# Kernel tuning notes

Measured on AMD Instinct MI355X. Metric: run time of the kernel, lower is better.

## Reference

```python
import jax, jax.numpy as jnp
import numpy as np

DIM = 640
HEADS = 8
HEAD_DIM = 80
CROSS = 768
FF_INNER = 4 * DIM  # 2560
EPS = 1e-5
SCALE = HEAD_DIM ** -0.5


def _ln(x, w, b):
    m = jnp.mean(x, axis=-1, keepdims=True)
    v = jnp.var(x, axis=-1, keepdims=True)
    return (x - m) * jax.lax.rsqrt(v + EPS) * w + b


def _split_heads(x):  # [B,S,D] -> [B,H,S,dh]
    B, S, D = x.shape
    return x.reshape(B, S, HEADS, D // HEADS).transpose(0, 2, 1, 3)


def _merge_heads(x):  # [B,H,S,dh] -> [B,S,D]
    B, H, S, dh = x.shape
    return x.transpose(0, 2, 1, 3).reshape(B, S, H * dh)


def _mha(q, k, v):
    # q:[B,S,D] k,v:[B,Skv,D]
    qh, kh, vh = _split_heads(q), _split_heads(k), _split_heads(v)
    scores = jnp.einsum('bhqd,bhkd->bhqk', qh, kh) * SCALE
    probs = jax.nn.softmax(scores, axis=-1)
    out = jnp.einsum('bhqk,bhkd->bhqd', probs, vh)
    return _merge_heads(out)


def _forward(hidden_states, encoder_hidden_states, video_length, p):
    BF, S, D = hidden_states.shape
    f = video_length
    b = BF // f

    # ---- attn1: sparse causal self-attention ----
    x = _ln(hidden_states, p['ln1_w'], p['ln1_b'])
    q = x @ p['q1']
    k = x @ p['k1']
    v = x @ p['v1']
    former = jnp.concatenate([jnp.zeros((1,), jnp.int32), jnp.arange(f - 1, dtype=jnp.int32)])
    def gather_kv(t):  # [BF,S,D] -> [BF,2S,D]
        t = t.reshape(b, f, S, D)
        first = jnp.broadcast_to(t[:, 0:1], (b, f, S, D))
        prev = t[:, former]
        return jnp.concatenate([first, prev], axis=2).reshape(BF, 2 * S, D)
    k = gather_kv(k)
    v = gather_kv(v)
    attn1 = _mha(q, k, v) @ p['o1_w'] + p['o1_b']
    hidden_states = attn1 + hidden_states

    # ---- attn2: cross attention to text ----
    x = _ln(hidden_states, p['ln2_w'], p['ln2_b'])
    q = x @ p['q2']
    k = encoder_hidden_states @ p['k2']
    v = encoder_hidden_states @ p['v2']
    attn2 = _mha(q, k, v) @ p['o2_w'] + p['o2_b']
    hidden_states = attn2 + hidden_states

    # ---- feed-forward (geglu) ----
    x = _ln(hidden_states, p['ln3_w'], p['ln3_b'])
    proj = x @ p['ff_w1'] + p['ff_b1']
    h, gate = jnp.split(proj, 2, axis=-1)
    ff = (h * jax.nn.gelu(gate)) @ p['ff_w2'] + p['ff_b2']
    return ff + hidden_states


def setup_inputs() -> dict:
    key = jax.random.key(0)
    ks = jax.random.split(key, 20)
    s = lambda i, shape, scale=0.02: jax.random.normal(ks[i], shape, jnp.float32) * scale
    inp = {
        'hidden_states': jax.random.normal(ks[0], (8, 1024, DIM), jnp.float32),
        'encoder_hidden_states': jax.random.normal(ks[1], (8, 77, CROSS), jnp.float32),
        'video_length': 8,
        'ln1_w': jnp.ones((DIM,)), 'ln1_b': jnp.zeros((DIM,)),
        'q1': s(2, (DIM, DIM)), 'k1': s(3, (DIM, DIM)), 'v1': s(4, (DIM, DIM)),
        'o1_w': s(5, (DIM, DIM)), 'o1_b': jnp.zeros((DIM,)),
        'ln2_w': jnp.ones((DIM,)), 'ln2_b': jnp.zeros((DIM,)),
        'q2': s(6, (DIM, DIM)), 'k2': s(7, (CROSS, DIM)), 'v2': s(8, (CROSS, DIM)),
        'o2_w': s(9, (DIM, DIM)), 'o2_b': jnp.zeros((DIM,)),
        'ln3_w': jnp.ones((DIM,)), 'ln3_b': jnp.zeros((DIM,)),
        'ff_w1': s(10, (DIM, 2 * FF_INNER)), 'ff_b1': jnp.zeros((2 * FF_INNER,)),
        'ff_w2': s(11, (FF_INNER, DIM)), 'ff_b2': jnp.zeros((DIM,)),
    }
    return inp


def reference(hidden_states, encoder_hidden_states, video_length,
              ln1_w, ln1_b, q1, k1, v1, o1_w, o1_b,
              ln2_w, ln2_b, q2, k2, v2, o2_w, o2_b,
              ln3_w, ln3_b, ff_w1, ff_b1, ff_w2, ff_b2):
    p = dict(ln1_w=ln1_w, ln1_b=ln1_b, q1=q1, k1=k1, v1=v1, o1_w=o1_w, o1_b=o1_b,
             ln2_w=ln2_w, ln2_b=ln2_b, q2=q2, k2=k2, v2=v2, o2_w=o2_w, o2_b=o2_b,
             ln3_w=ln3_w, ln3_b=ln3_b, ff_w1=ff_w1, ff_b1=ff_b1, ff_w2=ff_w2, ff_b2=ff_b2)
    return _forward(hidden_states, encoder_hidden_states, video_length, p)
```

## Files before the change

### kernel.cpp

```cpp
#include <hip/hip_runtime.h>
#include <stdint.h>

#define TOK   8192
#define DIM   640
#define HEADS 8
#define HD    80
#define SEQ   1024
#define CROSS 768
#define ETOK  616
#define FFI   2560
#define SCALE 0.11180339887498949f

typedef unsigned short u16;
typedef unsigned int   u32;

using bf8   = __attribute__((ext_vector_type(8))) short;
using f32x4 = __attribute__((ext_vector_type(4))) float;

struct __align__(16) U4 { u32 x, y, z, w; };
struct __align__(8)  U2 { u32 x, y; };

__device__ __forceinline__ float bf2f(u16 u){
  union { u32 i; float f; } v; v.i = ((u32)u) << 16; return v.f;
}
__device__ __forceinline__ u16 f2bf(float f){
  union { float f; u32 i; } v; v.f = f;
  u32 r = v.i + 0x7fffu + ((v.i >> 16) & 1u);
  return (u16)(r >> 16);
}
__device__ __forceinline__ u32 cvtpk_bf16(float lo, float hi){
  u32 r; asm("v_cvt_pk_bf16_f32 %0, %1, %2" : "=v"(r) : "v"(lo), "v"(hi)); return r;
}
__device__ __forceinline__ float gelu_t(float x){
  float y = 0.7978845608028654f * (x + 0.044715f * x * x * x);
  float e = __expf(2.f * y);
  return 0.5f * x * (2.f - 2.f / (e + 1.f));
}

__device__ __forceinline__ void gl2lds16(const u16* g, u16* l){
  __builtin_amdgcn_global_load_lds(
      (const __attribute__((address_space(1))) void*)g,
      (__attribute__((address_space(3))) void*)l, 16, 0, 0);
}

__global__ void zero_k(u16* p){ p[threadIdx.x] = 0; }

struct CvtJob  { const float* s; u16* d; int n; };
struct CvtJobs { CvtJob j[11]; };
__global__ __launch_bounds__(256) void cvt_all(CvtJobs jobs)
{
  const CvtJob jb = jobs.j[blockIdx.y];
  for (long i = (long)blockIdx.x*256 + threadIdx.x; i < jb.n; i += (long)gridDim.x*256)
    jb.d[i] = f2bf(jb.s[i]);
}

struct TJob  { const float* s; u16* d; int R, C, srcLd, dstLd; };
struct TJobs { TJob j[10]; };
__global__ __launch_bounds__(256) void transpose_tiled(TJobs jobs)
{
  const TJob jb = jobs.j[blockIdx.y];
  const int tilesC = jb.C >> 6;
  const int nt = (jb.R >> 6) * tilesC;
  if ((int)blockIdx.x >= nt) return;
  const int tr = (blockIdx.x / tilesC) << 6, tc = (blockIdx.x % tilesC) << 6;
  __shared__ u16 t[64][65];
  const int tid = threadIdx.x;
  const int rr = tid >> 3, c8 = (tid & 7) * 8;
  #pragma unroll
  for (int p = 0; p < 2; ++p){
    const int r = rr + p*32;
    const float* s = &jb.s[(long)(tr + r)*jb.srcLd + tc + c8];
    #pragma unroll
    for (int j = 0; j < 8; ++j) t[r][c8 + j] = f2bf(s[j]);
  }
  __syncthreads();
  #pragma unroll
  for (int p = 0; p < 2; ++p){
    const int c = rr + p*32;
    u16 tmp[8];
    #pragma unroll
    for (int j = 0; j < 8; ++j) tmp[j] = t[c8 + j][c];
    *(U4*)&jb.d[(long)(tc + c)*jb.dstLd + tr + c8] = *(U4*)tmp;
  }
}

__global__ __launch_bounds__(256) void transpose_tile(
    const u16* __restrict__ src, u16* __restrict__ dst,
    int srcLd, int dstLd)
{
  __shared__ u16 t[64][65];
  const int tr = blockIdx.y << 6, tc = blockIdx.x << 6;
  const int tid = threadIdx.x;
  const int rr = tid >> 3, c8 = (tid & 7) * 8;
  #pragma unroll
  for (int p = 0; p < 2; ++p){
    const int r = rr + p*32;
    U4 v = *(const U4*)&src[(long)(tr + r)*srcLd + tc + c8];
    const u16* pv = (const u16*)&v;
    #pragma unroll
    for (int j = 0; j < 8; ++j) t[r][c8 + j] = pv[j];
  }
  __syncthreads();
  #pragma unroll
  for (int p = 0; p < 2; ++p){
    const int c = rr + p*32;
    u16 tmp[8];
    #pragma unroll
    for (int j = 0; j < 8; ++j) tmp[j] = t[c8 + j][c];
    *(U4*)&dst[(long)(tc + c)*dstLd + tr + c8] = *(U4*)tmp;
  }
}

__global__ __launch_bounds__(256) void transpose_v2(
    const u16* __restrict__ src, u16* __restrict__ dst)
{
  int idx = blockIdx.x*256 + threadIdx.x;
  if (idx >= DIM*640) return;
  int d = idx / 640, c = idx - d*640;
  int g = c / 80, j = c - g*80;
  u16 v = 0;
  if (j < 77) v = src[(long)(g*77 + j)*(2*DIM) + DIM + d];
  dst[(long)d*640 + c] = v;
}

__global__ __launch_bounds__(256) void ln_k(
    const void* __restrict__ src, const u16* __restrict__ w,
    const u16* __restrict__ b, u16* __restrict__ dst, int srcf32)
{
  __shared__ float xr[DIM];
  __shared__ float red[256];
  const int tid = threadIdx.x;
  const long row = blockIdx.x;
  float ls = 0.f;
  for (int i = tid; i < DIM; i += 256){
    float v = srcf32 ? ((const float*)src)[row*DIM + i]
                     : bf2f(((const u16*)src)[row*DIM + i]);
    xr[i] = v; ls += v;
  }
  red[tid] = ls; __syncthreads();
  for (int o = 128; o > 0; o >>= 1){ if (tid < o) red[tid] += red[tid+o]; __syncthreads(); }
  const float mean = red[0] * (1.f/DIM);
  __syncthreads();
  float lq = 0.f;
  for (int i = tid; i < DIM; i += 256){ float d = xr[i] - mean; lq += d*d; }
  red[tid] = lq; __syncthreads();
  for (int o = 128; o > 0; o >>= 1){ if (tid < o) red[tid] += red[tid+o]; __syncthreads(); }
  const float var = red[0] * (1.f/DIM);
  const float rs = rsqrtf(var + 1e-5f);
  u16* q = dst + row*DIM;
  for (int i = tid; i < DIM; i += 256)
    q[i] = f2bf((xr[i] - mean)*rs*bf2f(w[i]) + bf2f(b[i]));
}

template<int BN>
__global__ __launch_bounds__(256) void gemm_bt(
    const u16* __restrict__ A, const u16* __restrict__ BT, void* __restrict__ C,
    int M, int N, int K, int lda, int ldb, int ldc,
    const u16* __restrict__ bias, const void* __restrict__ res, int ldr,
    int resf32, int outf32)
{
  constexpr int NT  = BN/32;
  constexpr int BCH = BN/16;
  constexpr int BPW = BCH/4;
  __shared__ __align__(16) u16 sA[2][8*512];
  __shared__ __align__(16) u16 sB[2][BCH*512];
  const int tid  = threadIdx.x;
  const int wave = tid >> 6, lane = tid & 63;
  const int quad = lane >> 4, l16 = lane & 15;
  const int m0 = blockIdx.y * 128, n0 = blockIdx.x * BN;
  const int wm = (wave >> 1) * 64, wn = (wave & 1) * (BN/2);
  const int srow = lane & 15;
  const int scol = (lane >> 4) * 8;

  long aoff[2];
  #pragma unroll
  for (int i = 0; i < 2; ++i){
    int r = m0 + (wave*2 + i)*16 + srow;
    r = r < M ? r : M - 1;
    aoff[i] = (long)r*lda + scol;
  }
  long boff[BPW];
  #pragma unroll
  for (int i = 0; i < BPW; ++i){
    int r = n0 + (wave*BPW + i)*16 + srow;
    boff[i] = (long)r*ldb + scol;
  }

  f32x4 acc[4][NT] = {};
  #pragma unroll
  for (int i = 0; i < 2; ++i)   gl2lds16(&A[aoff[i]],  &sA[0][(wave*2 + i)*512]);
  #pragma unroll
  for (int i = 0; i < BPW; ++i) gl2lds16(&BT[boff[i]], &sB[0][(wave*BPW + i)*512]);
  __syncthreads();

  int cur = 0;
  for (int k0 = 0; ; ){
    const int kn = k0 + 32;
    if (kn < K){
      #pragma unroll
      for (int i = 0; i < 2; ++i)   gl2lds16(&A[aoff[i] + kn],  &sA[cur^1][(wave*2 + i)*512]);
      #pragma unroll
      for (int i = 0; i < BPW; ++i) gl2lds16(&BT[boff[i] + kn], &sB[cur^1][(wave*BPW + i)*512]);
    }
    bf8 a[4], b[NT];
    #pragma unroll
    for (int mt = 0; mt < 4; ++mt)  a[mt] = *(const bf8*)&sA[cur][((wm>>4) + mt)*512 + lane*8];
    #pragma unroll
    for (int nt = 0; nt < NT; ++nt) b[nt] = *(const bf8*)&sB[cur][((wn>>4) + nt)*512 + lane*8];
    #pragma unroll
    for (int mt = 0; mt < 4; ++mt)
      #pragma unroll
      for (int nt = 0; nt < NT; ++nt)
        acc[mt][nt] = __builtin_amdgcn_mfma_f32_16x16x32_bf16(a[mt], b[nt], acc[mt][nt], 0, 0, 0);
    k0 = kn;
    if (k0 >= K) break;
    __syncthreads();
    cur ^= 1;
  }
  #pragma unroll
  for (int mt = 0; mt < 4; ++mt){
    const int rl = wm + mt*16 + quad*4;
    #pragma unroll
    for (int nt = 0; nt < NT; ++nt){
      const int col = n0 + wn + nt*16 + l16;
      float bv = bias ? bf2f(bias[col]) : 0.f;
      #pragma unroll
      for (int r = 0; r < 4; ++r){
        int row = m0 + rl + r;
        if (row < M){
          float v = acc[mt][nt][r] + bv;
          if (res) v += resf32 ? ((const float*)res)[(long)row*ldr + col]
                               : bf2f(((const u16*)res)[(long)row*ldr + col]);
          if (outf32) ((float*)C)[(long)row*ldc + col] = v;
          else        ((u16*)C) [(long)row*ldc + col] = f2bf(v);
        }
      }
    }
  }
}

__global__ __launch_bounds__(256) void gemm_geglu(
    const u16* __restrict__ A, const u16* __restrict__ W, u16* __restrict__ C,
    const u16* __restrict__ bias)
{
  __shared__ __align__(16) u16 sA[2][8*512];
  __shared__ __align__(16) u16 sH[2][4*512];
  __shared__ __align__(16) u16 sG[2][4*512];
  const int tid  = threadIdx.x;
  const int wave = tid >> 6, lane = tid & 63;
  const int quad = lane >> 4, l16 = lane & 15;
  const int m0 = blockIdx.y * 128, n0 = blockIdx.x * 64;
  const int wm = (wave >> 1) * 64, wn = (wave & 1) * 32;
  const int srow = lane & 15;
  const int scol = (lane >> 4) * 8;

  long aoff[2];
  #pragma unroll
  for (int i = 0; i < 2; ++i)
    aoff[i] = (long)(m0 + (wave*2 + i)*16 + srow)*DIM + scol;
  const long hoff = (long)(n0 + wave*16 + srow)*DIM + scol;
  const long goff = (long)(FFI + n0 + wave*16 + srow)*DIM + scol;

  f32x4 ah[4][2] = {}, ag[4][2] = {};
  #pragma unroll
  for (int i = 0; i < 2; ++i) gl2lds16(&A[aoff[i]], &sA[0][(wave*2 + i)*512]);
  gl2lds16(&W[hoff], &sH[0][wave*512]);
  gl2lds16(&W[goff], &sG[0][wave*512]);
  __syncthreads();

  int cur = 0;
  for (int k0 = 0; ; ){
    const int kn = k0 + 32;
    if (kn < DIM){
      #pragma unroll
      for (int i = 0; i < 2; ++i) gl2lds16(&A[aoff[i] + kn], &sA[cur^1][(wave*2 + i)*512]);
      gl2lds16(&W[hoff + kn], &sH[cur^1][wave*512]);
      gl2lds16(&W[goff + kn], &sG[cur^1][wave*512]);
    }
    bf8 a[4];
    #pragma unroll
    for (int mt = 0; mt < 4; ++mt) a[mt] = *(const bf8*)&sA[cur][((wm>>4) + mt)*512 + lane*8];
    #pragma unroll
    for (int nt = 0; nt < 2; ++nt){
      bf8 bh = *(const bf8*)&sH[cur][((wn>>4) + nt)*512 + lane*8];
      bf8 bg = *(const bf8*)&sG[cur][((wn>>4) + nt)*512 + lane*8];
      #pragma unroll
      for (int mt = 0; mt < 4; ++mt){
        ah[mt][nt] = __builtin_amdgcn_mfma_f32_16x16x32_bf16(a[mt], bh, ah[mt][nt], 0, 0, 0);
        ag[mt][nt] = __builtin_amdgcn_mfma_f32_16x16x32_bf16(a[mt], bg, ag[mt][nt], 0, 0, 0);
      }
    }
    k0 = kn;
    if (k0 >= DIM) break;
    __syncthreads();
    cur ^= 1;
  }
  #pragma unroll
  for (int mt = 0; mt < 4; ++mt){
    const int rl = wm + mt*16 + quad*4;
    #pragma unroll
    for (int nt = 0; nt < 2; ++nt){
      const int col = n0 + wn + nt*16 + l16;
      const float bh = bf2f(bias[col]);
      const float bg = bf2f(bias[FFI + col]);
      #pragma unroll
      for (int r = 0; r < 4; ++r){
        int row = m0 + rl + r;
        float h = ah[mt][nt][r] + bh;
        float g = ag[mt][nt][r] + bg;
        C[(long)row*FFI + col] = f2bf(h * gelu_t(g));
      }
    }
  }
}

template<int MODE>
__global__ __launch_bounds__(256) void attn_k(
    const u16* __restrict__ qbuf, const u16* __restrict__ kbuf,
    const u16* __restrict__ vT, u16* __restrict__ out,
    const u16* __restrict__ zblk)
{
  constexpr int QLD  = MODE ? DIM      : 3*DIM;
  constexpr int KLD  = MODE ? 2*DIM    : 3*DIM;
  constexpr int KCOL = MODE ? 0        : DIM;
  constexpr int VLD  = MODE ? DIM      : TOK;
  constexpr int NK   = MODE ? 77       : 2*SEQ;
  constexpr int NCH  = MODE ? 3        : 64;
  constexpr float C1   = SCALE * 1.4426950408889634f;
  constexpr float THRR = 8.0f / C1;

  const int qt = blockIdx.x, h = blockIdx.y, g = blockIdx.z;
  const int tid = threadIdx.x, wave = tid >> 6, lane = tid & 63;
  const int quad = lane >> 4, l16 = lane & 15;

  __shared__ __align__(16) u16 Qs[64*104];
  __shared__ __align__(16) u16 Kb[6*512];
  __shared__ __align__(16) u16 Vb[5*512];
  __shared__ __align__(16) u16 Ps[4][16*40];

  const int qrow0 = g*SEQ + qt*64;
  for (int v = tid; v < 640; v += 256){
    int r = v/10, c8 = (v - r*10)*8;
    *(U4*)&Qs[r*104 + c8] = *(const U4*)&qbuf[(long)(qrow0 + r)*QLD + h*HD + c8];
  }
  for (int v = tid; v < 128; v += 256){
    U4 z = {0,0,0,0};
    *(U4*)&Qs[(v>>1)*104 + 80 + (v&1)*8] = z;
  }
  __syncthreads();

  bf8 qf[3];
  #pragma unroll
  for (int ks = 0; ks < 3; ++ks)
    qf[ks] = *(const bf8*)&Qs[(wave*16 + l16)*104 + ks*32 + quad*8];

  const int former = (g == 0) ? 0 : (g - 1);

  auto stage = [&](int c){
    int krow0, vrow0;
    if (MODE == 0){
      int kb = c*32;
      int fr = (kb >> 10) ? former : 0;
      krow0 = fr*SEQ + (kb & (SEQ-1));
      vrow0 = krow0;
    } else {
      krow0 = c*32;
      vrow0 = g*80 + c*32;
    }
    #pragma unroll
    for (int ci = 0; ci < 6; ++ci){
      if ((ci & 3) == wave){
        const int ck = ci / 3, ks = ci % 3;
        const int d  = ks*32 + quad*8;
        const int rl = ck*16 + l16;
        const u16* src;
        if (MODE == 0){
          src = (d < HD) ? &kbuf[(long)(krow0 + rl)*KLD + KCOL + h*HD + d] : zblk;
        } else {
          int j = krow0 + rl; j = j < NK ? j : NK-1;
          src = (d < HD) ? &kbuf[((long)g*77 + j)*KLD + KCOL + h*HD + d] : zblk;
        }
        gl2lds16(src, &Kb[ci*512]);
      }
    }
    #pragma unroll
    for (int vi = 0; vi < 5; ++vi){
      if (((vi + 2) & 3) == wave){
        const int dd = vi*16 + l16;
        const u16* src;
        if (MODE == 0){
          src = &vT[(long)(h*HD + dd)*VLD + vrow0 + quad*8];
        } else {
          int key = c*32 + quad*8;
          src = (key < 80) ? &vT[(long)(h*HD + dd)*VLD + vrow0 + quad*8] : zblk;
        }
        gl2lds16(src, &Vb[vi*512]);
      }
    }
  };

  f32x4 o[5] = {};
  float mrun = -1e30f, lrun = 0.f, nmc = 0.f;

  for (int c = 0; c < NCH; ++c){
    stage(c);
    asm volatile("s_waitcnt vmcnt(0)" ::: "memory");
    __syncthreads();

    f32x4 s0 = {}, s1 = {};
    #pragma unroll
    for (int ks = 0; ks < 3; ++ks){
      bf8 kf0 = *(const bf8*)&Kb[ks*512     + lane*8];
      bf8 kf1 = *(const bf8*)&Kb[(3+ks)*512 + lane*8];
      s0 = __builtin_amdgcn_mfma_f32_16x16x32_bf16(kf0, qf[ks], s0, 0, 0, 0);
      s1 = __builtin_amdgcn_mfma_f32_16x16x32_bf16(kf1, qf[ks], s1, 0, 0, 0);
    }

    const int kbase = c*32;
    if (MODE == 1){
      const int kg = kbase + quad*4;
      #pragma unroll
      for (int r = 0; r < 4; ++r){
        if (kg + r >= NK)      s0[r] = -1e30f;
        if (kg + 16 + r >= NK) s1[r] = -1e30f;
      }
    }
    float mxs = fmaxf(fmaxf(fmaxf(s0[0],s0[1]), fmaxf(s0[2],s0[3])),
                      fmaxf(fmaxf(s1[0],s1[1]), fmaxf(s1[2],s1[3])));
    mxs = fmaxf(mxs, __shfl_xor(mxs, 16, 64));
    mxs = fmaxf(mxs, __shfl_xor(mxs, 32, 64));
    if (!__all(mxs - mrun <= THRR)){
      float mn = fmaxf(mrun, mxs);
      float al = exp2f((mrun - mn)*C1);
      mrun = mn; nmc = -mrun*C1;
      lrun *= al;
      float a0 = __shfl(al, quad*4 + 0, 16);
      float a1 = __shfl(al, quad*4 + 1, 16);
      float a2 = __shfl(al, quad*4 + 2, 16);
      float a3 = __shfl(al, quad*4 + 3, 16);
      #pragma unroll
      for (int dt = 0; dt < 5; ++dt){
        o[dt][0] *= a0; o[dt][1] *= a1; o[dt][2] *= a2; o[dt][3] *= a3;
      }
    }
    #pragma unroll
    for (int r = 0; r < 4; ++r){
      s0[r] = exp2f(__builtin_fmaf(s0[r], C1, nmc));
      s1[r] = exp2f(__builtin_fmaf(s1[r], C1, nmc));
    }
    float rs = ((s0[0]+s0[1])+(s0[2]+s0[3])) + ((s1[0]+s1[1])+(s1[2]+s1[3]));
    rs += __shfl_xor(rs, 16, 64);
    rs += __shfl_xor(rs, 32, 64);
    lrun += rs;

    U2 w01, w23;
    w01.x = cvtpk_bf16(s0[0], s0[1]);  w01.y = cvtpk_bf16(s0[2], s0[3]);
    w23.x = cvtpk_bf16(s1[0], s1[1]);  w23.y = cvtpk_bf16(s1[2], s1[3]);
    U2* pr = (U2*)&Ps[wave][l16*40];
    pr[quad]     = w01;
    pr[4 + quad] = w23;
    asm volatile("s_waitcnt lgkmcnt(0)" ::: "memory");
    __builtin_amdgcn_sched_barrier(0);
    bf8 pf = *(const bf8*)&Ps[wave][l16*40 + quad*8];
    #pragma unroll
    for (int dt = 0; dt < 5; ++dt){
      bf8 vf = *(const bf8*)&Vb[dt*512 + lane*8];
      o[dt] = __builtin_amdgcn_mfma_f32_16x16x32_bf16(pf, vf, o[dt], 0, 0, 0);
    }
    __syncthreads();
  }

  float linv[4];
  #pragma unroll
  for (int r = 0; r < 4; ++r)
    linv[r] = __builtin_amdgcn_rcpf(__shfl(lrun, quad*4 + r, 16));
  const int orow0 = qrow0 + wave*16 + quad*4;
  #pragma unroll
  for (int dt = 0; dt < 5; ++dt){
    const int col = h*HD + dt*16 + l16;
    #pragma unroll
    for (int r = 0; r < 4; ++r)
      out[(long)(orow0 + r)*DIM + col] = f2bf(o[dt][r] * linv[r]);
  }
}

extern "C" void kernel_launch(void* const* d_in, const int* in_sizes, int n_in,
                              void* d_out, int out_size, void* d_ws, size_t ws_size,
                              hipStream_t stream)
{
  const float* hidden = (const float*)d_in[0];
  const float* enc    = (const float*)d_in[1];
  const float* ln1w = (const float*)d_in[3],  *ln1b = (const float*)d_in[4];
  const float* q1   = (const float*)d_in[5],  *k1   = (const float*)d_in[6];
  const float* v1   = (const float*)d_in[7],  *o1w  = (const float*)d_in[8];
  const float* o1b  = (const float*)d_in[9];
  const float* ln2w = (const float*)d_in[10], *ln2b = (const float*)d_in[11];
  const float* q2   = (const float*)d_in[12], *k2   = (const float*)d_in[13];
  const float* v2   = (const float*)d_in[14], *o2w  = (const float*)d_in[15];
  const float* o2b  = (const float*)d_in[16];
  const float* ln3w = (const float*)d_in[17], *ln3b = (const float*)d_in[18];
  const float* fw1  = (const float*)d_in[19], *fb1  = (const float*)d_in[20];
  const float* fw2  = (const float*)d_in[21], *fb2  = (const float*)d_in[22];

  u16* ws = (u16*)d_ws;
  u16* Wqkv1T = ws;
  u16* o1T    = Wqkv1T + 1920*640;
  u16* q2T    = o1T    + 640*640;
  u16* Wkv2T  = q2T    + 640*640;
  u16* o2T    = Wkv2T  + 1280*768;
  u16* W1T    = o2T    + 640*640;
  u16* W2T    = W1T    + 5120*640;
  u16* xbuf   = W2T    + 640*2560;
  u16* qkv1   = xbuf   + (size_t)TOK*DIM;
  u16* v1T    = qkv1   + (size_t)TOK*3*DIM;
  u16* ffin   = qkv1;
  u16* attnb  = v1T    + (size_t)DIM*TOK;
  u16* hid2   = attnb  + (size_t)TOK*DIM;
  u16* hid3   = hid2   + (size_t)TOK*DIM;
  u16* q2buf  = hid3   + (size_t)TOK*DIM;
  u16* kv2    = q2buf  + (size_t)TOK*DIM;
  u16* v2T    = kv2    + (size_t)ETOK*2*DIM;
  u16* encm   = v2T    + 640*640 + 64;
  u16* bln1w  = encm   + (size_t)ETOK*CROSS;
  u16* bln1b  = bln1w + DIM;
  u16* bo1b   = bln1b + DIM;
  u16* bln2w  = bo1b  + DIM;
  u16* bln2b  = bln2w + DIM;
  u16* bo2b   = bln2b + DIM;
  u16* bln3w  = bo2b  + DIM;
  u16* bln3b  = bln3w + DIM;
  u16* bfb2   = bln3b + DIM;
  u16* bfb1   = bfb2  + DIM;
  u16* zblk   = bfb1  + 2*FFI;
  u16* wsend  = zblk  + 64;
  const size_t needed = ((size_t)(wsend - ws) + 64) * 2;
  if (ws_size < needed) return;

  dim3 blk(256);
  zero_k<<<1, 64, 0, stream>>>(zblk);

  CvtJobs jobs;
  jobs.j[0]  = { enc,  encm,  ETOK*CROSS };
  jobs.j[1]  = { ln1w, bln1w, DIM };
  jobs.j[2]  = { ln1b, bln1b, DIM };
  jobs.j[3]  = { o1b,  bo1b,  DIM };
  jobs.j[4]  = { ln2w, bln2w, DIM };
  jobs.j[5]  = { ln2b, bln2b, DIM };
  jobs.j[6]  = { o2b,  bo2b,  DIM };
  jobs.j[7]  = { ln3w, bln3w, DIM };
  jobs.j[8]  = { ln3b, bln3b, DIM };
  jobs.j[9]  = { fb2,  bfb2,  DIM };
  jobs.j[10] = { fb1,  bfb1,  2*FFI };
  cvt_all<<<dim3(64,11), blk, 0, stream>>>(jobs);

  TJobs tj;
  tj.j[0] = { q1,  Wqkv1T,            640, 640,  640,  640 };
  tj.j[1] = { k1,  Wqkv1T + 640*640,  640, 640,  640,  640 };
  tj.j[2] = { v1,  Wqkv1T + 1280*640, 640, 640,  640,  640 };
  tj.j[3] = { o1w, o1T,               640, 640,  640,  640 };
  tj.j[4] = { q2,  q2T,               640, 640,  640,  640 };
  tj.j[5] = { k2,  Wkv2T,             768, 640,  640,  768 };
  tj.j[6] = { v2,  Wkv2T + 640*768,   768, 640,  640,  768 };
  tj.j[7] = { o2w, o2T,               640, 640,  640,  640 };
  tj.j[8] = { fw1, W1T,               640, 5120, 5120, 640 };
  tj.j[9] = { fw2, W2T,               2560,640,  640,  2560 };
  transpose_tiled<<<dim3(800,10), blk, 0, stream>>>(tj);

  ln_k<<<TOK, blk, 0, stream>>>(hidden, bln1w, bln1b, xbuf, 1);
  gemm_bt<128><<<dim3(15,64), blk, 0, stream>>>(xbuf, Wqkv1T, qkv1,
      TOK, 3*DIM, DIM, DIM, DIM, 3*DIM, nullptr, nullptr, 0, 0, 0);
  transpose_tile<<<dim3(10,128), blk, 0, stream>>>(qkv1 + 2*DIM, v1T, 3*DIM, TOK);
  attn_k<0><<<dim3(16,8,8), blk, 0, stream>>>(qkv1, qkv1, v1T, attnb, zblk);
  gemm_bt<64><<<dim3(10,64), blk, 0, stream>>>(attnb, o1T, hid2,
      TOK, DIM, DIM, DIM, DIM, DIM, bo1b, hidden, DIM, 1, 0);

  ln_k<<<TOK, blk, 0, stream>>>(hid2, bln2w, bln2b, xbuf, 0);
  gemm_bt<64><<<dim3(10,64), blk, 0, stream>>>(xbuf, q2T, q2buf,
      TOK, DIM, DIM, DIM, DIM, DIM, nullptr, nullptr, 0, 0, 0);
  gemm_bt<64><<<dim3(20,5), blk, 0, stream>>>(encm, Wkv2T, kv2,
      ETOK, 2*DIM, CROSS, CROSS, CROSS, 2*DIM, nullptr, nullptr, 0, 0, 0);
  transpose_v2<<<dim3((DIM*640 + 255)/256), blk, 0, stream>>>(kv2, v2T);
  attn_k<1><<<dim3(16,8,8), blk, 0, stream>>>(q2buf, kv2, v2T, attnb, zblk);
  gemm_bt<64><<<dim3(10,64), blk, 0, stream>>>(attnb, o2T, hid3,
      TOK, DIM, DIM, DIM, DIM, DIM, bo2b, hid2, DIM, 0, 0);

  ln_k<<<TOK, blk, 0, stream>>>(hid3, bln3w, bln3b, xbuf, 0);
  gemm_geglu<<<dim3(40,64), blk, 0, stream>>>(xbuf, W1T, ffin, bfb1);
  gemm_bt<64><<<dim3(10,64), blk, 0, stream>>>(ffin, W2T, d_out,
      TOK, DIM, FFI, FFI, FFI, DIM, bfb2, hid3, DIM, 0, 1);
}
```

Before: 726.3 us.

## Double-buffer attention K/V staging and use wave-per-row LayerNorm

The attention kernel now issues the global-to-LDS copy of the next K/V chunk into a second buffer before computing on the current chunk. This is meant to hide load latency behind the MFMA and softmax work, and it drops the explicit vmcnt wait before the barrier. Q fragments are loaded straight from global memory into registers instead of going through LDS. LayerNorm switches to one wave per row with register-resident values, vectorized loads and shuffle reductions, replacing block-wide LDS tree reductions and quartering the grid. The risk is a race on the async LDS loads if the barrier does not wait on outstanding vector memory operations; LDS use also roughly doubles for K/V.

```diff
diff --git a/kernel.cpp b/kernel.cpp
--- a/kernel.cpp
+++ b/kernel.cpp
@@ -127,29 +127,47 @@
     const void* __restrict__ src, const u16* __restrict__ w,
     const u16* __restrict__ b, u16* __restrict__ dst, int srcf32)
 {
-  __shared__ float xr[DIM];
-  __shared__ float red[256];
-  const int tid = threadIdx.x;
-  const long row = blockIdx.x;
-  float ls = 0.f;
-  for (int i = tid; i < DIM; i += 256){
-    float v = srcf32 ? ((const float*)src)[row*DIM + i]
-                     : bf2f(((const u16*)src)[row*DIM + i]);
-    xr[i] = v; ls += v;
-  }
-  red[tid] = ls; __syncthreads();
-  for (int o = 128; o > 0; o >>= 1){ if (tid < o) red[tid] += red[tid+o]; __syncthreads(); }
-  const float mean = red[0] * (1.f/DIM);
-  __syncthreads();
-  float lq = 0.f;
-  for (int i = tid; i < DIM; i += 256){ float d = xr[i] - mean; lq += d*d; }
-  red[tid] = lq; __syncthreads();
-  for (int o = 128; o > 0; o >>= 1){ if (tid < o) red[tid] += red[tid+o]; __syncthreads(); }
-  const float var = red[0] * (1.f/DIM);
-  const float rs = rsqrtf(var + 1e-5f);
+  const int wave = threadIdx.x >> 6, lane = threadIdx.x & 63;
+  const long row = (long)blockIdx.x*4 + wave;
+  float x[10];
+  if (srcf32){
+    const float* s = (const float*)src + row*DIM;
+    #pragma unroll
+    for (int j = 0; j < 5; ++j){
+      float2 v = *(const float2*)&s[lane*2 + j*128];
+      x[j*2] = v.x; x[j*2+1] = v.y;
+    }
+  } else {
+    const u16* s = (const u16*)src + row*DIM;
+    #pragma unroll
+    for (int j = 0; j < 5; ++j){
+      u32 v = *(const u32*)&s[lane*2 + j*128];
+      x[j*2]   = bf2f((u16)(v & 0xffffu));
+      x[j*2+1] = bf2f((u16)(v >> 16));
+    }
+  }
+  float sum = 0.f;
+  #pragma unroll
+  for (int i = 0; i < 10; ++i) sum += x[i];
+  #pragma unroll
+  for (int d = 1; d < 64; d <<= 1) sum += __shfl_xor(sum, d, 64);
+  const float mean = sum * (1.f/DIM);
+  float vq = 0.f;
+  #pragma unroll
+  for (int i = 0; i < 10; ++i){ float dd = x[i] - mean; vq += dd*dd; }
+  #pragma unroll
+  for (int d = 1; d < 64; d <<= 1) vq += __shfl_xor(vq, d, 64);
+  const float rs = rsqrtf(vq * (1.f/DIM) + 1e-5f);
   u16* q = dst + row*DIM;
-  for (int i = tid; i < DIM; i += 256)
-    q[i] = f2bf((xr[i] - mean)*rs*bf2f(w[i]) + bf2f(b[i]));
+  #pragma unroll
+  for (int j = 0; j < 5; ++j){
+    const int off = lane*2 + j*128;
+    u32 wv = *(const u32*)&w[off];
+    u32 bv = *(const u32*)&b[off];
+    float o0 = (x[j*2]   - mean)*rs*bf2f((u16)(wv & 0xffffu)) + bf2f((u16)(bv & 0xffffu));
+    float o1 = (x[j*2+1] - mean)*rs*bf2f((u16)(wv >> 16))     + bf2f((u16)(bv >> 16));
+    *(u32*)&q[off] = (u32)f2bf(o0) | ((u32)f2bf(o1) << 16);
+  }
 }
 
 template<int BN>
@@ -333,39 +351,30 @@
   const int tid = threadIdx.x, wave = tid >> 6, lane = tid & 63;
   const int quad = lane >> 4, l16 = lane & 15;
 
-  __shared__ __align__(16) u16 Qs[64*104];
-  __shared__ __align__(16) u16 Kb[6*512];
-  __shared__ __align__(16) u16 Vb[5*512];
+  __shared__ __align__(16) u16 Kb[2][6*512];
+  __shared__ __align__(16) u16 Vb[2][5*512];
   __shared__ __align__(16) u16 Ps[4][16*40];
 
   const int qrow0 = g*SEQ + qt*64;
-  for (int v = tid; v < 640; v += 256){
-    int r = v/10, c8 = (v - r*10)*8;
-    *(U4*)&Qs[r*104 + c8] = *(const U4*)&qbuf[(long)(qrow0 + r)*QLD + h*HD + c8];
-  }
-  for (int v = tid; v < 128; v += 256){
-    U4 z = {0,0,0,0};
-    *(U4*)&Qs[(v>>1)*104 + 80 + (v&1)*8] = z;
-  }
-  __syncthreads();
-
   bf8 qf[3];
-  #pragma unroll
-  for (int ks = 0; ks < 3; ++ks)
-    qf[ks] = *(const bf8*)&Qs[(wave*16 + l16)*104 + ks*32 + quad*8];
+  {
+    const long qbase = (long)(qrow0 + wave*16 + l16)*QLD + h*HD;
+    #pragma unroll
+    for (int ks = 0; ks < 3; ++ks){
+      const int d = ks*32 + quad*8;
+      const u16* src = (d < HD) ? &qbuf[qbase + d] : zblk;
+      qf[ks] = *(const bf8*)src;
+    }
+  }
 
   const int former = (g == 0) ? 0 : (g - 1);
 
-  auto stage = [&](int c){
-    int krow0, vrow0;
+  auto stage = [&](int c, int buf){
+    int krow0 = 0;
     if (MODE == 0){
       int kb = c*32;
       int fr = (kb >> 10) ? former : 0;
       krow0 = fr*SEQ + (kb & (SEQ-1));
-      vrow0 = krow0;
-    } else {
-      krow0 = c*32;
-      vrow0 = g*80 + c*32;
     }
     #pragma unroll
     for (int ci = 0; ci < 6; ++ci){
@@ -377,10 +386,10 @@
         if (MODE == 0){
           src = (d < HD) ? &kbuf[(long)(krow0 + rl)*KLD + KCOL + h*HD + d] : zblk;
         } else {
-          int j = krow0 + rl; j = j < NK ? j : NK-1;
+          int j = c*32 + rl; j = j < NK ? j : NK-1;
           src = (d < HD) ? &kbuf[((long)g*77 + j)*KLD + KCOL + h*HD + d] : zblk;
         }
-        gl2lds16(src, &Kb[ci*512]);
+        gl2lds16(src, &Kb[buf][ci*512]);
       }
     }
     #pragma unroll
@@ -389,12 +398,12 @@
         const int dd = vi*16 + l16;
         const u16* src;
         if (MODE == 0){
-          src = &vT[(long)(h*HD + dd)*VLD + vrow0 + quad*8];
+          src = &vT[(long)(h*HD + dd)*VLD + krow0 + quad*8];
         } else {
           int key = c*32 + quad*8;
-          src = (key < 80) ? &vT[(long)(h*HD + dd)*VLD + vrow0 + quad*8] : zblk;
+          src = (key < 80) ? &vT[(long)(h*HD + dd)*VLD + g*80 + key] : zblk;
         }
-        gl2lds16(src, &Vb[vi*512]);
+        gl2lds16(src, &Vb[buf][vi*512]);
       }
     }
   };
@@ -402,16 +411,18 @@
   f32x4 o[5] = {};
   float mrun = -1e30f, lrun = 0.f, nmc = 0.f;
 
+  stage(0, 0);
+  __syncthreads();
+  int cur = 0;
+
   for (int c = 0; c < NCH; ++c){
-    stage(c);
-    asm volatile("s_waitcnt vmcnt(0)" ::: "memory");
-    __syncthreads();
+    if (c + 1 < NCH) stage(c + 1, cur ^ 1);
 
     f32x4 s0 = {}, s1 = {};
     #pragma unroll
     for (int ks = 0; ks < 3; ++ks){
-      bf8 kf0 = *(const bf8*)&Kb[ks*512     + lane*8];
-      bf8 kf1 = *(const bf8*)&Kb[(3+ks)*512 + lane*8];
+      bf8 kf0 = *(const bf8*)&Kb[cur][ks*512     + lane*8];
+      bf8 kf1 = *(const bf8*)&Kb[cur][(3+ks)*512 + lane*8];
       s0 = __builtin_amdgcn_mfma_f32_16x16x32_bf16(kf0, qf[ks], s0, 0, 0, 0);
       s1 = __builtin_amdgcn_mfma_f32_16x16x32_bf16(kf1, qf[ks], s1, 0, 0, 0);
     }
@@ -464,10 +475,11 @@
     bf8 pf = *(const bf8*)&Ps[wave][l16*40 + quad*8];
     #pragma unroll
     for (int dt = 0; dt < 5; ++dt){
-      bf8 vf = *(const bf8*)&Vb[dt*512 + lane*8];
+      bf8 vf = *(const bf8*)&Vb[cur][dt*512 + lane*8];
       o[dt] = __builtin_amdgcn_mfma_f32_16x16x32_bf16(pf, vf, o[dt], 0, 0, 0);
     }
     __syncthreads();
+    cur ^= 1;
   }
 
   float linv[4];
@@ -566,7 +578,7 @@
   tj.j[9] = { fw2, W2T,               2560,640,  640,  2560 };
   transpose_tiled<<<dim3(800,10), blk, 0, stream>>>(tj);
 
-  ln_k<<<TOK, blk, 0, stream>>>(hidden, bln1w, bln1b, xbuf, 1);
+  ln_k<<<TOK/4, blk, 0, stream>>>(hidden, bln1w, bln1b, xbuf, 1);
   gemm_bt<128><<<dim3(15,64), blk, 0, stream>>>(xbuf, Wqkv1T, qkv1,
       TOK, 3*DIM, DIM, DIM, DIM, 3*DIM, nullptr, nullptr, 0, 0, 0);
   transpose_tile<<<dim3(10,128), blk, 0, stream>>>(qkv1 + 2*DIM, v1T, 3*DIM, TOK);
@@ -574,7 +586,7 @@
   gemm_bt<64><<<dim3(10,64), blk, 0, stream>>>(attnb, o1T, hid2,
       TOK, DIM, DIM, DIM, DIM, DIM, bo1b, hidden, DIM, 1, 0);
 
-  ln_k<<<TOK, blk, 0, stream>>>(hid2, bln2w, bln2b, xbuf, 0);
+  ln_k<<<TOK/4, blk, 0, stream>>>(hid2, bln2w, bln2b, xbuf, 0);
   gemm_bt<64><<<dim3(10,64), blk, 0, stream>>>(xbuf, q2T, q2buf,
       TOK, DIM, DIM, DIM, DIM, DIM, nullptr, nullptr, 0, 0, 0);
   gemm_bt<64><<<dim3(20,5), blk, 0, stream>>>(encm, Wkv2T, kv2,
@@ -584,7 +596,7 @@
   gemm_bt<64><<<dim3(10,64), blk, 0, stream>>>(attnb, o2T, hid3,
       TOK, DIM, DIM, DIM, DIM, DIM, bo2b, hid2, DIM, 0, 0);
 
-  ln_k<<<TOK, blk, 0, stream>>>(hid3, bln3w, bln3b, xbuf, 0);
+  ln_k<<<TOK/4, blk, 0, stream>>>(hid3, bln3w, bln3b, xbuf, 0);
   gemm_geglu<<<dim3(40,64), blk, 0, stream>>>(xbuf, W1T, ffin, bfb1);
   gemm_bt<64><<<dim3(10,64), blk, 0, stream>>>(ffin, W2T, d_out,
       TOK, DIM, FFI, FFI, FFI, DIM, bfb2, hid3, DIM, 0, 1);
```

Result: faster. 678.3 us (-6.6%).
